# Kernel tuning notes

Measured on AMD Instinct MI355X. Metric: run time of the kernel, lower is better.

The kernel has to match this reference:

```python
import jax, jax.numpy as jnp
import numpy as np

E = 300000
N_ATOMS = 10000
C = 256
RBF = 16
NUM_TARGET = 1


def setup_inputs() -> dict:
    key = jax.random.key(0)
    ks = jax.random.split(key, 12)
    s = lambda fan_in: 1.0 / np.sqrt(fan_in)
    return {
        "x": jax.random.normal(ks[0], (E, C), dtype=jnp.float32),
        "rbf": jax.random.uniform(ks[1], (E, RBF), dtype=jnp.float32),
        "num_atoms": N_ATOMS,
        "edge_index_0": jax.random.randint(ks[2], (E,), 0, N_ATOMS, dtype=jnp.int64),
        # lin_rbf: Linear(rbf_dim -> in_channels)
        "w_rbf": jax.random.normal(ks[3], (C, RBF), dtype=jnp.float32) * s(RBF),
        "b_rbf": jnp.zeros((C,), dtype=jnp.float32),
        # mlp: Linear(C,C), SiLU, Linear(C,C), SiLU, Linear(C, num_target)
        "w1": jax.random.normal(ks[4], (C, C), dtype=jnp.float32) * s(C),
        "b1": jnp.zeros((C,), dtype=jnp.float32),
        "w2": jax.random.normal(ks[5], (C, C), dtype=jnp.float32) * s(C),
        "b2": jnp.zeros((C,), dtype=jnp.float32),
        "w3": jax.random.normal(ks[6], (NUM_TARGET, C), dtype=jnp.float32) * s(C),
        "b3": jnp.zeros((NUM_TARGET,), dtype=jnp.float32),
    }


def reference(x, rbf, num_atoms, edge_index_0, w_rbf, b_rbf, w1, b1, w2, b2, w3, b3):
    # rbf_filter = lin_rbf(rbf): [E, C]
    rbf_filter = rbf @ w_rbf.T + b_rbf
    msg = rbf_filter * x  # [E, C]
    # scatter_add over edge source -> per-atom features [num_atoms, C]
    out = jax.ops.segment_sum(msg, edge_index_0, num_segments=num_atoms)
    # MLP: Linear+SiLU, Linear+SiLU, Linear
    out = jax.nn.silu(out @ w1.T + b1)
    out = jax.nn.silu(out @ w2.T + b2)
    out = out @ w3.T + b3  # [num_atoms, num_target]
    return out
```

## Files before the change

### kernel.cpp

```cpp
#include <hip/hip_runtime.h>
#include <math.h>

#define CDIM 256
#define RBFD 16
#define NATOMS 10000

__device__ __forceinline__ float dot4f(float4 a, float4 b) {
  return a.x * b.x + a.y * b.y + a.z * b.z + a.w * b.w;
}

__global__ void hist_kernel(const int* __restrict__ eidx, int* __restrict__ counts,
                            int E) {
  const int i = blockIdx.x * blockDim.x + threadIdx.x;
  if (i < E) atomicAdd(&counts[eidx[i]], 1);
}

__global__ void scan_kernel(const int* __restrict__ counts,
                            int* __restrict__ offsets, int* __restrict__ cursor) {
  __shared__ int part[256];
  const int t = threadIdx.x;
  const int CH = (NATOMS + 255) / 256;
  const int base = t * CH;
  const int n = min(CH, max(0, NATOMS - base));
  int s = 0;
  for (int j = 0; j < n; ++j) s += counts[base + j];
  part[t] = s;
  __syncthreads();
  for (int off = 1; off < 256; off <<= 1) {
    int v = 0;
    if (t >= off) v = part[t - off];
    __syncthreads();
    part[t] += v;
    __syncthreads();
  }
  int run = part[t] - s;
  for (int j = 0; j < n; ++j) {
    offsets[base + j] = run;
    cursor[base + j] = run;
    run += counts[base + j];
  }
  if (t == 255) offsets[NATOMS] = part[255];
}

__global__ void scatter_kernel(const int* __restrict__ eidx,
                               int* __restrict__ cursor, int* __restrict__ elist,
                               int E) {
  const int i = blockIdx.x * blockDim.x + threadIdx.x;
  if (i < E) {
    const int a = eidx[i];
    const int pos = atomicAdd(&cursor[a], 1);
    elist[pos] = i;
  }
}

__global__ __launch_bounds__(256, 4) void gather_kernel(
    const float* __restrict__ x, const float* __restrict__ rbf,
    const int* __restrict__ elist, const int* __restrict__ offsets,
    const float* __restrict__ w_rbf, const float* __restrict__ b_rbf,
    float* __restrict__ acc) {
  const int lane = threadIdx.x & 63;
  const int atom = (blockIdx.x * blockDim.x + threadIdx.x) >> 6;
  if (atom >= NATOMS) return;
  const int c0 = lane * 4;

  float4 wv[4][4];
  const float4 bb = *(const float4*)(b_rbf + c0);
#pragma unroll
  for (int j = 0; j < 4; ++j) {
    const float4* wr = (const float4*)(w_rbf + (size_t)(c0 + j) * RBFD);
    wv[j][0] = wr[0];
    wv[j][1] = wr[1];
    wv[j][2] = wr[2];
    wv[j][3] = wr[3];
  }

  const int start = offsets[atom];
  const int end = offsets[atom + 1];
  float4 sum = make_float4(0.f, 0.f, 0.f, 0.f);

  int e = (start < end) ? elist[start] : 0;
  for (int i = start; i < end; ++i) {
    const int e_next = (i + 1 < end) ? elist[i + 1] : 0;
    const float4* rp = (const float4*)(rbf + (size_t)e * RBFD);
    const float4 r0 = rp[0], r1 = rp[1], r2 = rp[2], r3 = rp[3];
    const float4 xx = *(const float4*)(x + (size_t)e * CDIM + c0);

    float4 f;
    f.x = bb.x + dot4f(wv[0][0], r0) + dot4f(wv[0][1], r1) +
          dot4f(wv[0][2], r2) + dot4f(wv[0][3], r3);
    f.y = bb.y + dot4f(wv[1][0], r0) + dot4f(wv[1][1], r1) +
          dot4f(wv[1][2], r2) + dot4f(wv[1][3], r3);
    f.z = bb.z + dot4f(wv[2][0], r0) + dot4f(wv[2][1], r1) +
          dot4f(wv[2][2], r2) + dot4f(wv[2][3], r3);
    f.w = bb.w + dot4f(wv[3][0], r0) + dot4f(wv[3][1], r1) +
          dot4f(wv[3][2], r2) + dot4f(wv[3][3], r3);

    sum.x += f.x * xx.x;
    sum.y += f.y * xx.y;
    sum.z += f.z * xx.z;
    sum.w += f.w * xx.w;
    e = e_next;
  }
  *(float4*)(acc + (size_t)atom * CDIM + c0) = sum;
}

__global__ void transpose_kernel(const float* __restrict__ w1,
                                 const float* __restrict__ w2,
                                 float* __restrict__ w1T,
                                 float* __restrict__ w2T) {
  __shared__ float tile[32][33];
  const float* src = blockIdx.z ? w2 : w1;
  float* dst = blockIdx.z ? w2T : w1T;
  const int bx = blockIdx.x * 32;
  const int by = blockIdx.y * 32;
  const int tx = threadIdx.x, ty = threadIdx.y;
#pragma unroll
  for (int i = 0; i < 32; i += 8)
    tile[ty + i][tx] = src[(size_t)(by + ty + i) * CDIM + bx + tx];
  __syncthreads();
#pragma unroll
  for (int i = 0; i < 32; i += 8)
    dst[(size_t)(bx + ty + i) * CDIM + by + tx] = tile[tx][ty + i];
}

__global__ __launch_bounds__(256, 2) void mlp_kernel(
    const float* __restrict__ hin, const float* __restrict__ w1T,
    const float* __restrict__ b1, const float* __restrict__ w2T,
    const float* __restrict__ b2, const float* __restrict__ w3,
    const float* __restrict__ b3, float* __restrict__ out, int natoms) {
  __shared__ float H[32 * 256];
  __shared__ float WK[32 * 256];
  const int tid = threadIdx.x;
  const int tc = tid & 31;
  const int ta = tid >> 5;
  const int a0 = blockIdx.x * 32;
  const int cA = tc * 4;
  const int cB = 128 + tc * 4;

  {
    const float4* src = (const float4*)hin + (size_t)a0 * 64;
    float4* Hv = (float4*)H;
#pragma unroll
    for (int i = 0; i < 8; ++i) {
      const int idx = tid + i * 256;
      const int ga = a0 + (idx >> 6);
      Hv[idx] = (ga < natoms) ? src[idx] : make_float4(0.f, 0.f, 0.f, 0.f);
    }
  }

  float s[4][8];

#pragma unroll 1
  for (int layer = 0; layer < 2; ++layer) {
    const float* wT = (layer == 0) ? w1T : w2T;
    const float* bias = (layer == 0) ? b1 : b2;
    float r[4][8];
    const float4 bA = *(const float4*)(bias + cA);
    const float4 bB = *(const float4*)(bias + cB);
#pragma unroll
    for (int a = 0; a < 4; ++a) {
      r[a][0] = bA.x; r[a][1] = bA.y; r[a][2] = bA.z; r[a][3] = bA.w;
      r[a][4] = bB.x; r[a][5] = bB.y; r[a][6] = bB.z; r[a][7] = bB.w;
    }

    for (int k0 = 0; k0 < 256; k0 += 32) {
      __syncthreads();
      {
        const float4* wsrc = (const float4*)(wT + (size_t)k0 * CDIM);
        float4* WKv = (float4*)WK;
#pragma unroll
        for (int i = 0; i < 8; ++i) WKv[tid + i * 256] = wsrc[tid + i * 256];
      }
      __syncthreads();

#pragma unroll
      for (int kk = 0; kk < 32; kk += 4) {
        float4 ha[4];
#pragma unroll
        for (int a = 0; a < 4; ++a)
          ha[a] = *(const float4*)&H[(ta * 4 + a) * 256 + k0 + kk];
#pragma unroll
        for (int u = 0; u < 4; ++u) {
          const float4 w0 = *(const float4*)&WK[(kk + u) * 256 + cA];
          const float4 w1v = *(const float4*)&WK[(kk + u) * 256 + cB];
#pragma unroll
          for (int a = 0; a < 4; ++a) {
            const float hv = (u == 0) ? ha[a].x
                           : (u == 1) ? ha[a].y
                           : (u == 2) ? ha[a].z : ha[a].w;
            r[a][0] += hv * w0.x;  r[a][1] += hv * w0.y;
            r[a][2] += hv * w0.z;  r[a][3] += hv * w0.w;
            r[a][4] += hv * w1v.x; r[a][5] += hv * w1v.y;
            r[a][6] += hv * w1v.z; r[a][7] += hv * w1v.w;
          }
        }
      }
    }

#pragma unroll
    for (int a = 0; a < 4; ++a)
#pragma unroll
      for (int j = 0; j < 8; ++j) {
        const float v = r[a][j];
        s[a][j] = v / (1.0f + __expf(-v));
      }

    if (layer == 0) {
      __syncthreads();
#pragma unroll
      for (int a = 0; a < 4; ++a) {
        *(float4*)&H[(ta * 4 + a) * 256 + cA] =
            make_float4(s[a][0], s[a][1], s[a][2], s[a][3]);
        *(float4*)&H[(ta * 4 + a) * 256 + cB] =
            make_float4(s[a][4], s[a][5], s[a][6], s[a][7]);
      }
    }
  }

  const float4 w3a = *(const float4*)(w3 + cA);
  const float4 w3b = *(const float4*)(w3 + cB);
  float part[4];
#pragma unroll
  for (int a = 0; a < 4; ++a) {
    part[a] = s[a][0] * w3a.x + s[a][1] * w3a.y + s[a][2] * w3a.z +
              s[a][3] * w3a.w + s[a][4] * w3b.x + s[a][5] * w3b.y +
              s[a][6] * w3b.z + s[a][7] * w3b.w;
  }
  __syncthreads();
  float* red = WK;
#pragma unroll
  for (int a = 0; a < 4; ++a) red[(ta * 4 + a) * 33 + tc] = part[a];
  __syncthreads();
  if (tid < 32) {
    float sum = 0.f;
#pragma unroll
    for (int j = 0; j < 32; ++j) sum += red[tid * 33 + j];
    const int ga = a0 + tid;
    if (ga < natoms) out[ga] = sum + b3[0];
  }
}

extern "C" void kernel_launch(void* const* d_in, const int* in_sizes, int n_in,
                              void* d_out, int out_size, void* d_ws,
                              size_t ws_size, hipStream_t stream) {
  const float* x = (const float*)d_in[0];
  const float* rbf = (const float*)d_in[1];
  const int* eidx = (const int*)d_in[3];
  const float* w_rbf = (const float*)d_in[4];
  const float* b_rbf = (const float*)d_in[5];
  const float* w1 = (const float*)d_in[6];
  const float* b1 = (const float*)d_in[7];
  const float* w2 = (const float*)d_in[8];
  const float* b2 = (const float*)d_in[9];
  const float* w3 = (const float*)d_in[10];
  const float* b3 = (const float*)d_in[11];
  float* out = (float*)d_out;
  const int E = in_sizes[0] / CDIM;

  char* p = (char*)d_ws;
  float* acc = (float*)p;              p += (size_t)NATOMS * CDIM * sizeof(float);
  float* w1T = (float*)p;              p += CDIM * CDIM * sizeof(float);
  float* w2T = (float*)p;              p += CDIM * CDIM * sizeof(float);
  int* counts = (int*)p;               p += NATOMS * sizeof(int);
  int* offsets = (int*)p;              p += (NATOMS + 1) * sizeof(int);
  int* cursor = (int*)p;               p += NATOMS * sizeof(int);
  int* elist = (int*)p;                p += (size_t)E * sizeof(int);

  hipMemsetAsync(counts, 0, NATOMS * sizeof(int), stream);
  hist_kernel<<<(E + 255) / 256, 256, 0, stream>>>(eidx, counts, E);
  scan_kernel<<<1, 256, 0, stream>>>(counts, offsets, cursor);
  scatter_kernel<<<(E + 255) / 256, 256, 0, stream>>>(eidx, cursor, elist, E);
  transpose_kernel<<<dim3(8, 8, 2), dim3(32, 8), 0, stream>>>(w1, w2, w1T, w2T);
  gather_kernel<<<(NATOMS * 64 + 255) / 256, 256, 0, stream>>>(
      x, rbf, elist, offsets, w_rbf, b_rbf, acc);
  mlp_kernel<<<(NATOMS + 31) / 32, 256, 0, stream>>>(acc, w1T, b1, w2T, b2, w3,
                                                     b3, out, NATOMS);
}
```

Baseline: 662.3 us.

## Split each atom's edges across four waves and shrink MLP weight tiles

```diff
diff --git a/kernel.cpp b/kernel.cpp
--- a/kernel.cpp
+++ b/kernel.cpp
@@ -58,13 +58,15 @@
     const int* __restrict__ elist, const int* __restrict__ offsets,
     const float* __restrict__ w_rbf, const float* __restrict__ b_rbf,
     float* __restrict__ acc) {
-  const int lane = threadIdx.x & 63;
-  const int atom = (blockIdx.x * blockDim.x + threadIdx.x) >> 6;
-  if (atom >= NATOMS) return;
+  __shared__ float partial[4][256];
+  __shared__ int eids[4][64];
+  const int tid = threadIdx.x;
+  const int lane = tid & 63;
+  const int w = tid >> 6;
+  const int atom = blockIdx.x;
   const int c0 = lane * 4;
 
   float4 wv[4][4];
-  const float4 bb = *(const float4*)(b_rbf + c0);
 #pragma unroll
   for (int j = 0; j < 4; ++j) {
     const float4* wr = (const float4*)(w_rbf + (size_t)(c0 + j) * RBFD);
@@ -78,30 +80,56 @@
   const int end = offsets[atom + 1];
   float4 sum = make_float4(0.f, 0.f, 0.f, 0.f);
 
-  int e = (start < end) ? elist[start] : 0;
-  for (int i = start; i < end; ++i) {
-    const int e_next = (i + 1 < end) ? elist[i + 1] : 0;
-    const float4* rp = (const float4*)(rbf + (size_t)e * RBFD);
-    const float4 r0 = rp[0], r1 = rp[1], r2 = rp[2], r3 = rp[3];
-    const float4 xx = *(const float4*)(x + (size_t)e * CDIM + c0);
-
-    float4 f;
-    f.x = bb.x + dot4f(wv[0][0], r0) + dot4f(wv[0][1], r1) +
-          dot4f(wv[0][2], r2) + dot4f(wv[0][3], r3);
-    f.y = bb.y + dot4f(wv[1][0], r0) + dot4f(wv[1][1], r1) +
-          dot4f(wv[1][2], r2) + dot4f(wv[1][3], r3);
-    f.z = bb.z + dot4f(wv[2][0], r0) + dot4f(wv[2][1], r1) +
-          dot4f(wv[2][2], r2) + dot4f(wv[2][3], r3);
-    f.w = bb.w + dot4f(wv[3][0], r0) + dot4f(wv[3][1], r1) +
-          dot4f(wv[3][2], r2) + dot4f(wv[3][3], r3);
-
-    sum.x += f.x * xx.x;
-    sum.y += f.y * xx.y;
-    sum.z += f.z * xx.z;
-    sum.w += f.w * xx.w;
-    e = e_next;
-  }
-  *(float4*)(acc + (size_t)atom * CDIM + c0) = sum;
+  for (int base = start + w * 64; base < end; base += 256) {
+    const int n = min(64, end - base);
+    if (lane < n) eids[w][lane] = elist[base + lane];
+    int e = eids[w][0];
+    float4 xx = *(const float4*)(x + (size_t)e * CDIM + c0);
+    const float* rp = rbf + (size_t)e * RBFD;
+    float4 r0 = *(const float4*)rp, r1 = *(const float4*)(rp + 4),
+           r2 = *(const float4*)(rp + 8), r3 = *(const float4*)(rp + 12);
+    for (int j = 0; j < n; ++j) {
+      const float4 cx = xx, c0v = r0, c1v = r1, c2v = r2, c3v = r3;
+      if (j + 1 < n) {
+        e = eids[w][j + 1];
+        xx = *(const float4*)(x + (size_t)e * CDIM + c0);
+        const float* rq = rbf + (size_t)e * RBFD;
+        r0 = *(const float4*)rq;
+        r1 = *(const float4*)(rq + 4);
+        r2 = *(const float4*)(rq + 8);
+        r3 = *(const float4*)(rq + 12);
+      }
+      float4 f;
+      f.x = dot4f(wv[0][0], c0v) + dot4f(wv[0][1], c1v) +
+            dot4f(wv[0][2], c2v) + dot4f(wv[0][3], c3v);
+      f.y = dot4f(wv[1][0], c0v) + dot4f(wv[1][1], c1v) +
+            dot4f(wv[1][2], c2v) + dot4f(wv[1][3], c3v);
+      f.z = dot4f(wv[2][0], c0v) + dot4f(wv[2][1], c1v) +
+            dot4f(wv[2][2], c2v) + dot4f(wv[2][3], c3v);
+      f.w = dot4f(wv[3][0], c0v) + dot4f(wv[3][1], c1v) +
+            dot4f(wv[3][2], c2v) + dot4f(wv[3][3], c3v);
+      const float4 bb = *(const float4*)(b_rbf + c0);
+      sum.x += (bb.x + f.x) * cx.x;
+      sum.y += (bb.y + f.y) * cx.y;
+      sum.z += (bb.z + f.z) * cx.z;
+      sum.w += (bb.w + f.w) * cx.w;
+    }
+  }
+
+  *(float4*)&partial[w][c0] = sum;
+  __syncthreads();
+  if (w == 0) {
+    const float4 p0 = *(const float4*)&partial[0][c0];
+    const float4 p1 = *(const float4*)&partial[1][c0];
+    const float4 p2 = *(const float4*)&partial[2][c0];
+    const float4 p3 = *(const float4*)&partial[3][c0];
+    float4 tot;
+    tot.x = (p0.x + p1.x) + (p2.x + p3.x);
+    tot.y = (p0.y + p1.y) + (p2.y + p3.y);
+    tot.z = (p0.z + p1.z) + (p2.z + p3.z);
+    tot.w = (p0.w + p1.w) + (p2.w + p3.w);
+    *(float4*)(acc + (size_t)atom * CDIM + c0) = tot;
+  }
 }
 
 __global__ void transpose_kernel(const float* __restrict__ w1,
@@ -123,13 +151,13 @@
     dst[(size_t)(bx + ty + i) * CDIM + by + tx] = tile[tx][ty + i];
 }
 
-__global__ __launch_bounds__(256, 2) void mlp_kernel(
+__global__ __launch_bounds__(256, 3) void mlp_kernel(
     const float* __restrict__ hin, const float* __restrict__ w1T,
     const float* __restrict__ b1, const float* __restrict__ w2T,
     const float* __restrict__ b2, const float* __restrict__ w3,
     const float* __restrict__ b3, float* __restrict__ out, int natoms) {
   __shared__ float H[32 * 256];
-  __shared__ float WK[32 * 256];
+  __shared__ float WK[16 * 256];
   const int tid = threadIdx.x;
   const int tc = tid & 31;
   const int ta = tid >> 5;
@@ -163,18 +191,18 @@
       r[a][4] = bB.x; r[a][5] = bB.y; r[a][6] = bB.z; r[a][7] = bB.w;
     }
 
-    for (int k0 = 0; k0 < 256; k0 += 32) {
+    for (int k0 = 0; k0 < 256; k0 += 16) {
       __syncthreads();
       {
         const float4* wsrc = (const float4*)(wT + (size_t)k0 * CDIM);
         float4* WKv = (float4*)WK;
 #pragma unroll
-        for (int i = 0; i < 8; ++i) WKv[tid + i * 256] = wsrc[tid + i * 256];
+        for (int i = 0; i < 4; ++i) WKv[tid + i * 256] = wsrc[tid + i * 256];
       }
       __syncthreads();
 
 #pragma unroll
-      for (int kk = 0; kk < 32; kk += 4) {
+      for (int kk = 0; kk < 16; kk += 4) {
         float4 ha[4];
 #pragma unroll
         for (int a = 0; a < 4; ++a)
@@ -266,13 +294,13 @@
   int* cursor = (int*)p;               p += NATOMS * sizeof(int);
   int* elist = (int*)p;                p += (size_t)E * sizeof(int);
 
-  hipMemsetAsync(counts, 0, NATOMS * sizeof(int), stream);
+  (void)hipMemsetAsync(counts, 0, NATOMS * sizeof(int), stream);
   hist_kernel<<<(E + 255) / 256, 256, 0, stream>>>(eidx, counts, E);
   scan_kernel<<<1, 256, 0, stream>>>(counts, offsets, cursor);
   scatter_kernel<<<(E + 255) / 256, 256, 0, stream>>>(eidx, cursor, elist, E);
   transpose_kernel<<<dim3(8, 8, 2), dim3(32, 8), 0, stream>>>(w1, w2, w1T, w2T);
-  gather_kernel<<<(NATOMS * 64 + 255) / 256, 256, 0, stream>>>(
-      x, rbf, elist, offsets, w_rbf, b_rbf, acc);
+  gather_kernel<<<NATOMS, 256, 0, stream>>>(x, rbf, elist, offsets, w_rbf,
+                                            b_rbf, acc);
   mlp_kernel<<<(NATOMS + 31) / 32, 256, 0, stream>>>(acc, w1T, b1, w2T, b2, w3,
                                                      b3, out, NATOMS);
 }
```

Result: slower. 1.347 ms (+103.4%).
